# Kernel optimization log

Measured on AMD Instinct MI355X. Metric: run time of the kernel, lower is better.

The kernel has to match this reference:

```python
import jax, jax.numpy as jnp
import numpy as np

B, S, D, H = 4, 2048, 768, 12
HD = D // H  # head_dim = 64


def setup_inputs() -> dict:
    key = jax.random.key(0)
    ks = jax.random.split(key, 5)
    scale = 0.02
    return {
        "x": jax.random.normal(ks[0], (B, S, D), dtype=jnp.float32),
        "wq": jax.random.normal(ks[1], (D, D), dtype=jnp.float32) * scale,
        "wk": jax.random.normal(ks[2], (D, D), dtype=jnp.float32) * scale,
        "wv": jax.random.normal(ks[3], (D, D), dtype=jnp.float32) * scale,
        "wo": jax.random.normal(ks[4], (D, D), dtype=jnp.float32) * scale,
        "bo": jnp.zeros((D,), dtype=jnp.float32),
    }


def reference(x, wq, wk, wv, wo, bo):
    b, s, d = x.shape
    # torch Linear: y = x @ W.T ; qkv_bias=False
    q = (x @ wq.T).reshape(b, s, H, HD).transpose(0, 2, 1, 3)  # [b,h,s,hd]
    k = (x @ wk.T).reshape(b, s, H, HD).transpose(0, 2, 1, 3)
    v = (x @ wv.T).reshape(b, s, H, HD).transpose(0, 2, 1, 3)
    scores = jnp.einsum("bhqd,bhkd->bhqk", q, k)  # full [b,h,s,s] score matrix
    causal = jnp.triu(jnp.ones((s, s), dtype=bool), k=1)
    scores = jnp.where(causal, -jnp.inf, scores)
    attn = jax.nn.softmax(scores / jnp.sqrt(jnp.float32(HD)), axis=-1)
    ctx = jnp.einsum("bhqk,bhkd->bhqd", attn, v)
    ctx = ctx.transpose(0, 2, 1, 3).reshape(b, s, d)
    return ctx @ wo.T + bo  # dropout is identity in eval mode
```

## Files before the change

kernel.cpp:

```cpp
#include <hip/hip_runtime.h>

#define H 12
#define S 2048
#define D 768
#define HD 64
#define BATCH 4
#define M_TOT (BATCH * S)

typedef __attribute__((ext_vector_type(8))) short bf16x8;
typedef __attribute__((ext_vector_type(4))) float f32x4;

__device__ __forceinline__ ushort f2bf(float f) {
  unsigned int x = __float_as_uint(f);
  x += 0x7fffu + ((x >> 16) & 1u);
  return (ushort)(x >> 16);
}

__device__ __forceinline__ uint cvt_pk_bf16(float lo, float hi) {
  uint r;
  asm("v_cvt_pk_bf16_f32 %0, %1, %2" : "=v"(r) : "v"(lo), "v"(hi));
  return r;
}

__device__ __forceinline__ void gload_lds16(const void* gsrc, void* lds) {
  __builtin_amdgcn_global_load_lds(
      (const __attribute__((address_space(1))) unsigned int*)gsrc,
      (__attribute__((address_space(3))) unsigned int*)lds, 16, 0, 0);
}

__global__ __launch_bounds__(256) void cast_all(
    const float* __restrict__ x, const float* __restrict__ wq,
    const float* __restrict__ wk, const float* __restrict__ wv,
    const float* __restrict__ wo, ushort* __restrict__ xb,
    ushort* __restrict__ wqb, ushort* __restrict__ wkb,
    ushort* __restrict__ wvb, ushort* __restrict__ wob) {
  const int NX = M_TOT * D / 4;
  const int NW = D * D / 4;
  int i = blockIdx.x * 256 + threadIdx.x;
  const float* src; ushort* dst; int off;
  if (i < NX) { src = x; dst = xb; off = i; }
  else {
    int j = i - NX; int w = j / NW; off = j - w * NW;
    src = (w == 0) ? wq : (w == 1) ? wk : (w == 2) ? wv : wo;
    dst = (w == 0) ? wqb : (w == 1) ? wkb : (w == 2) ? wvb : wob;
  }
  float4 f = reinterpret_cast<const float4*>(src)[off];
  ushort4 u;
  u.x = f2bf(f.x); u.y = f2bf(f.y); u.z = f2bf(f.z); u.w = f2bf(f.w);
  reinterpret_cast<ushort4*>(dst)[off] = u;
}

__global__ __launch_bounds__(256, 3) void gemm_qkv(
    const ushort* __restrict__ xb, const ushort* __restrict__ wqb,
    const ushort* __restrict__ wkb, const ushort* __restrict__ wvb,
    ushort* __restrict__ qb, ushort* __restrict__ kb_,
    ushort* __restrict__ vtb, float qscale) {
  __shared__ ushort SM[2][10240];
  const int tid = threadIdx.x;
  const int lane = tid & 63, wid = tid >> 6;
  const int g = lane >> 4, li = lane & 15;

  const int wg = blockIdx.x;
  const int mt = wg & 63, slab = wg >> 6;
  const int m0 = mt * 128, n0 = slab * 64;

  const ushort* xm = xb + (size_t)m0 * 768;
  const ushort* wqn = wqb + (size_t)n0 * 768;
  const ushort* wkn = wkb + (size_t)n0 * 768;
  const ushort* wvn = wvb + (size_t)n0 * 768;

  const int rsub = lane >> 2;
  const int coff = (((lane & 3) ^ ((rsub >> 1) & 3)) << 3);
  const int wrow = wid * 16;

  auto stage = [&](int buf, int k0) {
#pragma unroll
    for (int rnd = 0; rnd < 2; ++rnd) {
      const int row0 = rnd * 64 + wrow;
      gload_lds16(&xm[(size_t)(row0 + rsub) * 768 + k0 + coff], &SM[buf][row0 * 32]);
    }
    gload_lds16(&wqn[(size_t)(wrow + rsub) * 768 + k0 + coff], &SM[buf][4096 + wrow * 32]);
    gload_lds16(&wkn[(size_t)(wrow + rsub) * 768 + k0 + coff], &SM[buf][6144 + wrow * 32]);
    gload_lds16(&wvn[(size_t)(wrow + rsub) * 768 + k0 + coff], &SM[buf][8192 + wrow * 32]);
  };

  f32x4 acc[3][2][4] = {};
  stage(0, 0);

  for (int kt = 0; kt < 24; ++kt) {
    const int cur = kt & 1;
    asm volatile("s_waitcnt vmcnt(0)" ::: "memory");
    __syncthreads();
    if (kt + 1 < 24) stage(cur ^ 1, (kt + 1) * 32);

    const ushort* bp = &SM[cur][0];
    bf16x8 a[2];
#pragma unroll
    for (int i = 0; i < 2; ++i) {
      const int row = wid * 32 + i * 16 + li;
      a[i] = *reinterpret_cast<const bf16x8*>(
          &bp[row * 32 + ((g ^ ((row >> 1) & 3)) << 3)]);
    }
#pragma unroll
    for (int o = 0; o < 3; ++o) {
      const int off = 4096 + o * 2048;
      bf16x8 b[4];
#pragma unroll
      for (int j = 0; j < 4; ++j) {
        const int row = j * 16 + li;
        b[j] = *reinterpret_cast<const bf16x8*>(
            &bp[off + row * 32 + ((g ^ ((row >> 1) & 3)) << 3)]);
      }
      __builtin_amdgcn_s_setprio(1);
#pragma unroll
      for (int i = 0; i < 2; ++i)
#pragma unroll
        for (int j = 0; j < 4; ++j)
          acc[o][i][j] = __builtin_amdgcn_mfma_f32_16x16x32_bf16(a[i], b[j], acc[o][i][j], 0, 0, 0);
      __builtin_amdgcn_s_setprio(0);
    }
  }

  ushort* Cs = &SM[0][0];
  const int b0 = m0 >> 11, sb = m0 & 2047;

  __syncthreads();
#pragma unroll
  for (int o = 0; o < 2; ++o)
#pragma unroll
    for (int i = 0; i < 2; ++i)
#pragma unroll
      for (int j = 0; j < 4; ++j)
#pragma unroll
        for (int rr = 0; rr < 4; ++rr) {
          const int row = wid * 32 + i * 16 + g * 4 + rr;
          const int col = j * 16 + li;
          const int pc = ((((col >> 3) ^ (row & 7)) << 3) | (col & 7));
          const float v = acc[o][i][j][rr] * (o == 0 ? qscale : 1.0f);
          Cs[o * 8192 + row * 64 + pc] = f2bf(v);
        }
  __syncthreads();
  {
    const int row = tid >> 1, half = tid & 1;
    const int m = m0 + row;
    const size_t rb = (((size_t)b0 * H + slab) * S + (m & 2047)) * HD + half * 32;
    ushort* dq = &qb[rb];
    ushort* dk = &kb_[rb];
#pragma unroll
    for (int c8 = 0; c8 < 4; ++c8) {
      const int col = half * 32 + c8 * 8;
      const int chunk = (col >> 3) ^ (row & 7);
      *reinterpret_cast<bf16x8*>(&dq[c8 * 8]) =
          *reinterpret_cast<const bf16x8*>(&Cs[row * 64 + chunk * 8]);
      *reinterpret_cast<bf16x8*>(&dk[c8 * 8]) =
          *reinterpret_cast<const bf16x8*>(&Cs[8192 + row * 64 + chunk * 8]);
    }
  }

  __syncthreads();
#pragma unroll
  for (int i = 0; i < 2; ++i)
#pragma unroll
    for (int j = 0; j < 4; ++j)
#pragma unroll
      for (int rr = 0; rr < 4; ++rr) {
        const int tok = wid * 32 + i * 16 + g * 4 + rr;
        const int feat = j * 16 + li;
        const int pc = ((((tok >> 3) ^ (feat & 7)) << 3) | (tok & 7));
        Cs[feat * 128 + pc] = f2bf(acc[2][i][j][rr]);
      }
  __syncthreads();
  {
    const int feat = tid >> 2, qtr = tid & 3;
    ushort* dv = &vtb[(((size_t)b0 * H + slab) * HD + feat) * S + sb + qtr * 32];
#pragma unroll
    for (int c8 = 0; c8 < 4; ++c8) {
      const int tok = qtr * 32 + c8 * 8;
      const int chunk = (tok >> 3) ^ (feat & 7);
      *reinterpret_cast<bf16x8*>(&dv[c8 * 8]) =
          *reinterpret_cast<const bf16x8*>(&Cs[feat * 128 + chunk * 8]);
    }
  }
}

__global__ __launch_bounds__(256) void gemm_wo(const ushort* __restrict__ A,
                                               const ushort* __restrict__ W,
                                               float* __restrict__ out_f,
                                               const float* __restrict__ bias) {
  __shared__ ushort SM[3][6144];
  const int tid = threadIdx.x;
  const int lane = tid & 63, wid = tid >> 6;
  const int g = lane >> 4, li = lane & 15;
  const int wm = wid >> 1, wn = wid & 1;
  const int m0 = blockIdx.x * 64, n0 = blockIdx.y * 128;

  const int rsub = lane >> 2;
  const int coff = (((lane & 3) ^ ((rsub >> 1) & 3)) << 3);

  auto stage = [&](int buf, int k0) {
    gload_lds16(&A[(size_t)(m0 + wid * 16 + rsub) * 768 + k0 + coff],
                &SM[buf][wid * 16 * 32]);
#pragma unroll
    for (int rnd = 0; rnd < 2; ++rnd) {
      const int row0 = rnd * 64 + wid * 16;
      gload_lds16(&W[(size_t)(n0 + row0 + rsub) * 768 + k0 + coff],
                  &SM[buf][2048 + row0 * 32]);
    }
  };

  f32x4 acc[2][4] = {};
  stage(0, 0);
  stage(1, 32);

  int cur = 0, pre = 2;
  for (int kt = 0; kt < 24; ++kt) {
    if (kt < 23) asm volatile("s_waitcnt vmcnt(3) lgkmcnt(0)" ::: "memory");
    else         asm volatile("s_waitcnt vmcnt(0) lgkmcnt(0)" ::: "memory");
    __builtin_amdgcn_s_barrier();
    if (kt + 2 < 24) stage(pre, (kt + 2) * 32);

    bf16x8 a[2], b[4];
#pragma unroll
    for (int i = 0; i < 2; ++i) {
      const int row = wm * 32 + i * 16 + li;
      a[i] = *reinterpret_cast<const bf16x8*>(
          &SM[cur][row * 32 + ((g ^ ((row >> 1) & 3)) << 3)]);
    }
#pragma unroll
    for (int j = 0; j < 4; ++j) {
      const int row = wn * 64 + j * 16 + li;
      b[j] = *reinterpret_cast<const bf16x8*>(
          &SM[cur][2048 + row * 32 + ((g ^ ((row >> 1) & 3)) << 3)]);
    }
    __builtin_amdgcn_s_setprio(1);
#pragma unroll
    for (int i = 0; i < 2; ++i)
#pragma unroll
      for (int j = 0; j < 4; ++j)
        acc[i][j] = __builtin_amdgcn_mfma_f32_16x16x32_bf16(a[i], b[j], acc[i][j], 0, 0, 0);
    __builtin_amdgcn_s_setprio(0);

    cur = (cur == 2) ? 0 : cur + 1;
    pre = (pre == 2) ? 0 : pre + 1;
  }

#pragma unroll
  for (int i = 0; i < 2; ++i)
#pragma unroll
    for (int j = 0; j < 4; ++j)
#pragma unroll
      for (int r = 0; r < 4; ++r) {
        const int m = m0 + wm * 32 + i * 16 + g * 4 + r;
        const int n = n0 + wn * 64 + j * 16 + li;
        out_f[(size_t)m * 768 + n] = acc[i][j][r] + bias[n];
      }
}

__global__ __launch_bounds__(256) void attn_kernel(const ushort* __restrict__ Q,
                                                   const ushort* __restrict__ K,
                                                   const ushort* __restrict__ VT,
                                                   ushort* __restrict__ ctx) {
  __shared__ ushort Ks[2][64 * 64];
  __shared__ ushort Vts[2][64 * 64];
  __shared__ ushort Ps[4][32][72];

  const int tid = threadIdx.x;
  const int lane = tid & 63, wid = tid >> 6;
  const int g = lane >> 4, li = lane & 15;

  const int wg = blockIdx.x;
  const int xcd = wg & 7, t = wg >> 3;
  const int bh = xcd + 8 * (t >> 4);
  const int p = t & 15;
  const int qL = 64 * (31 - p), qS = 64 * p;

  const size_t base = (size_t)bh * S * HD;
  const size_t vtbase = (size_t)bh * HD * S;

  bf16x8 aq[2][2];
#pragma unroll
  for (int f = 0; f < 2; ++f) {
    const size_t qr = base + (size_t)((f ? qS : qL) + wid * 16 + li) * HD;
#pragma unroll
    for (int c = 0; c < 2; ++c)
      aq[f][c] = *reinterpret_cast<const bf16x8*>(&Q[qr + c * 32 + g * 8]);
  }

  f32x4 acc[2][4] = {};
  f32x4 accl[2] = {};
  const uint one2 = 0x3F803F80u;
  uint4 ouv = {one2, one2, one2, one2};
  const bf16x8 ones8 = *reinterpret_cast<const bf16x8*>(&ouv);

  const int nkt = 32 - p;

  const int rsub = lane >> 3;
  const int c8e = (((lane & 7) ^ rsub) << 3);

  auto stage = [&](int buf, int k0) {
#pragma unroll
    for (int rnd = 0; rnd < 2; ++rnd) {
      const int row0 = rnd * 32 + wid * 8;
      gload_lds16(&K[base + (size_t)(k0 + row0 + rsub) * HD + c8e], &Ks[buf][row0 << 6]);
      gload_lds16(&VT[vtbase + (size_t)(row0 + rsub) * S + k0 + c8e], &Vts[buf][row0 << 6]);
    }
  };

  stage(0, 0);

  for (int kt = 0; kt < nkt; ++kt) {
    const int cur = kt & 1;
    const int k0 = kt * 64;
    const bool doS = (kt <= p);

    asm volatile("s_waitcnt vmcnt(0)" ::: "memory");
    __syncthreads();
    if (kt + 1 < nkt) stage(cur ^ 1, k0 + 64);

    f32x4 sc[2][4];
    __builtin_amdgcn_s_setprio(1);
#pragma unroll
    for (int ct = 0; ct < 4; ++ct) {
      const int row = ct * 16 + li, r7 = row & 7;
      const ushort* kr = &Ks[cur][row << 6];
      bf16x8 kb0 = *reinterpret_cast<const bf16x8*>(&kr[(g ^ r7) << 3]);
      bf16x8 kb1 = *reinterpret_cast<const bf16x8*>(&kr[((4 + g) ^ r7) << 3]);
      {
        f32x4 z = {};
        z = __builtin_amdgcn_mfma_f32_16x16x32_bf16(kb0, aq[0][0], z, 0, 0, 0);
        z = __builtin_amdgcn_mfma_f32_16x16x32_bf16(kb1, aq[0][1], z, 0, 0, 0);
        sc[0][ct] = z;
      }
      if (doS) {
        f32x4 z = {};
        z = __builtin_amdgcn_mfma_f32_16x16x32_bf16(kb0, aq[1][0], z, 0, 0, 0);
        z = __builtin_amdgcn_mfma_f32_16x16x32_bf16(kb1, aq[1][1], z, 0, 0, 0);
        sc[1][ct] = z;
      }
    }
    __builtin_amdgcn_s_setprio(0);

    if (kt == nkt - 1) {
      const int q = qL + wid * 16 + li;
#pragma unroll
      for (int ct = 0; ct < 4; ++ct)
#pragma unroll
        for (int r = 0; r < 4; ++r)
          if (k0 + ct * 16 + 4 * g + r > q) sc[0][ct][r] = -1e30f;
    }
    if (kt == p) {
      const int q = qS + wid * 16 + li;
#pragma unroll
      for (int ct = 0; ct < 4; ++ct)
#pragma unroll
        for (int r = 0; r < 4; ++r)
          if (k0 + ct * 16 + 4 * g + r > q) sc[1][ct][r] = -1e30f;
    }

#pragma unroll
    for (int f = 0; f < 2; ++f) {
      if (f == 1 && !doS) break;
#pragma unroll
      for (int ct = 0; ct < 4; ++ct) {
        float p0 = __builtin_amdgcn_exp2f(sc[f][ct][0]);
        float p1 = __builtin_amdgcn_exp2f(sc[f][ct][1]);
        float p2 = __builtin_amdgcn_exp2f(sc[f][ct][2]);
        float p3 = __builtin_amdgcn_exp2f(sc[f][ct][3]);
        uint2 pw;
        pw.x = cvt_pk_bf16(p0, p1);
        pw.y = cvt_pk_bf16(p2, p3);
        *reinterpret_cast<uint2*>(&Ps[wid][f * 16 + li][ct * 16 + 4 * g]) = pw;
      }
    }

    bf16x8 pa[2][2];
    pa[0][0] = *reinterpret_cast<const bf16x8*>(&Ps[wid][li][g * 8]);
    pa[0][1] = *reinterpret_cast<const bf16x8*>(&Ps[wid][li][32 + g * 8]);
    if (doS) {
      pa[1][0] = *reinterpret_cast<const bf16x8*>(&Ps[wid][16 + li][g * 8]);
      pa[1][1] = *reinterpret_cast<const bf16x8*>(&Ps[wid][16 + li][32 + g * 8]);
    }
    __builtin_amdgcn_s_setprio(1);
    accl[0] = __builtin_amdgcn_mfma_f32_16x16x32_bf16(pa[0][0], ones8, accl[0], 0, 0, 0);
    accl[0] = __builtin_amdgcn_mfma_f32_16x16x32_bf16(pa[0][1], ones8, accl[0], 0, 0, 0);
    if (doS) {
      accl[1] = __builtin_amdgcn_mfma_f32_16x16x32_bf16(pa[1][0], ones8, accl[1], 0, 0, 0);
      accl[1] = __builtin_amdgcn_mfma_f32_16x16x32_bf16(pa[1][1], ones8, accl[1], 0, 0, 0);
    }
#pragma unroll
    for (int dt = 0; dt < 4; ++dt) {
      const int row = dt * 16 + li, r7 = row & 7;
      const ushort* vr = &Vts[cur][row << 6];
      bf16x8 vb0 = *reinterpret_cast<const bf16x8*>(&vr[(g ^ r7) << 3]);
      bf16x8 vb1 = *reinterpret_cast<const bf16x8*>(&vr[((4 + g) ^ r7) << 3]);
      acc[0][dt] = __builtin_amdgcn_mfma_f32_16x16x32_bf16(pa[0][0], vb0, acc[0][dt], 0, 0, 0);
      acc[0][dt] = __builtin_amdgcn_mfma_f32_16x16x32_bf16(pa[0][1], vb1, acc[0][dt], 0, 0, 0);
      if (doS) {
        acc[1][dt] = __builtin_amdgcn_mfma_f32_16x16x32_bf16(pa[1][0], vb0, acc[1][dt], 0, 0, 0);
        acc[1][dt] = __builtin_amdgcn_mfma_f32_16x16x32_bf16(pa[1][1], vb1, acc[1][dt], 0, 0, 0);
      }
    }
    __builtin_amdgcn_s_setprio(0);
  }

  const int b = bh / H, h = bh % H;
#pragma unroll
  for (int f = 0; f < 2; ++f) {
#pragma unroll
    for (int r = 0; r < 4; ++r) {
      const float inv = 1.0f / accl[f][r];
      const int s = (f ? qS : qL) + wid * 16 + 4 * g + r;
#pragma unroll
      for (int dt = 0; dt < 4; ++dt)
        ctx[((size_t)(b * S + s)) * D + h * HD + dt * 16 + li] =
            f2bf(acc[f][dt][r] * inv);
    }
  }
}

extern "C" void kernel_launch(void* const* d_in, const int* in_sizes, int n_in,
                              void* d_out, int out_size, void* d_ws, size_t ws_size,
                              hipStream_t stream) {
  (void)in_sizes; (void)n_in; (void)out_size; (void)ws_size;
  const float* x  = (const float*)d_in[0];
  const float* wq = (const float*)d_in[1];
  const float* wk = (const float*)d_in[2];
  const float* wv = (const float*)d_in[3];
  const float* wo = (const float*)d_in[4];
  const float* bo = (const float*)d_in[5];
  float* out = (float*)d_out;

  const size_t xn = (size_t)M_TOT * D;
  const size_t wn = (size_t)D * D;

  ushort* p = (ushort*)d_ws;
  ushort* x_bf  = p; p += xn;
  ushort* wq_bf = p; p += wn;
  ushort* wk_bf = p; p += wn;
  ushort* wv_bf = p; p += wn;
  ushort* wo_bf = p; p += wn;
  ushort* q_bf  = p; p += xn;
  ushort* k_bf  = p; p += xn;
  ushort* vt_bf = p; p += xn;
  ushort* ctx_bf = x_bf;

  cast_all<<<8448, 256, 0, stream>>>(x, wq, wk, wv, wo,
                                     x_bf, wq_bf, wk_bf, wv_bf, wo_bf);

  const float QSCALE = 0.125f * 1.44269504f;
  gemm_qkv<<<768, 256, 0, stream>>>(x_bf, wq_bf, wk_bf, wv_bf,
                                    q_bf, k_bf, vt_bf, QSCALE);

  attn_kernel<<<768, 256, 0, stream>>>(q_bf, k_bf, vt_bf, ctx_bf);

  gemm_wo<<<dim3(128, 6), 256, 0, stream>>>(ctx_bf, wo_bf, out, bo);
}
```

Before: 126.1 us.

## Merge two paired query-tile work items per 512-thread block sharing K/V staging

Attention blocks grow from 4 to 8 waves, and each block handles two adjacent long/short query-tile pairs that share the same K/V tiles staged in LDS. Each wave loads a single 8-row slice per stage instead of two, and waves skip the compute for key tiles beyond their own causal range. The intent is to halve K/V global traffic and staging per unit of work. In exchange, the grid is halved, the waves for the shorter pair sit idle on the final tile, and the P buffer is reused serially per fragment.

```diff
diff --git a/kernel.cpp b/kernel.cpp
--- a/kernel.cpp
+++ b/kernel.cpp
@@ -256,23 +256,31 @@
       }
 }
 
-__global__ __launch_bounds__(256) void attn_kernel(const ushort* __restrict__ Q,
+__global__ __launch_bounds__(512) void attn_kernel(const ushort* __restrict__ Q,
                                                    const ushort* __restrict__ K,
                                                    const ushort* __restrict__ VT,
                                                    ushort* __restrict__ ctx) {
   __shared__ ushort Ks[2][64 * 64];
   __shared__ ushort Vts[2][64 * 64];
-  __shared__ ushort Ps[4][32][72];
+  __shared__ ushort Ps[8][16][72];
 
   const int tid = threadIdx.x;
   const int lane = tid & 63, wid = tid >> 6;
   const int g = lane >> 4, li = lane & 15;
 
   const int wg = blockIdx.x;
-  const int xcd = wg & 7, t = wg >> 3;
-  const int bh = xcd + 8 * (t >> 4);
-  const int p = t & 15;
-  const int qL = 64 * (31 - p), qS = 64 * p;
+  const int xcd = wg & 7;
+  const int rest = wg >> 3;
+  const int headi = rest % 6;
+  const int k2 = rest / 6;
+  const int bh = headi * 8 + xcd;
+
+  const int pA = 2 * k2;
+  const int myp = pA + (wid >> 2);
+  const int qL = 64 * (31 - myp), qS = 64 * myp;
+  const int wr = (wid & 3) * 16;
+  const int myNkt = 32 - myp;
+  const int nkt = 32 - pA;
 
   const size_t base = (size_t)bh * S * HD;
   const size_t vtbase = (size_t)bh * HD * S;
@@ -280,7 +288,7 @@
   bf16x8 aq[2][2];
 #pragma unroll
   for (int f = 0; f < 2; ++f) {
-    const size_t qr = base + (size_t)((f ? qS : qL) + wid * 16 + li) * HD;
+    const size_t qr = base + (size_t)((f ? qS : qL) + wr + li) * HD;
 #pragma unroll
     for (int c = 0; c < 2; ++c)
       aq[f][c] = *reinterpret_cast<const bf16x8*>(&Q[qr + c * 32 + g * 8]);
@@ -292,18 +300,13 @@
   uint4 ouv = {one2, one2, one2, one2};
   const bf16x8 ones8 = *reinterpret_cast<const bf16x8*>(&ouv);
 
-  const int nkt = 32 - p;
-
   const int rsub = lane >> 3;
+  const int srow = wid * 8 + rsub;
   const int c8e = (((lane & 7) ^ rsub) << 3);
 
   auto stage = [&](int buf, int k0) {
-#pragma unroll
-    for (int rnd = 0; rnd < 2; ++rnd) {
-      const int row0 = rnd * 32 + wid * 8;
-      gload_lds16(&K[base + (size_t)(k0 + row0 + rsub) * HD + c8e], &Ks[buf][row0 << 6]);
-      gload_lds16(&VT[vtbase + (size_t)(row0 + rsub) * S + k0 + c8e], &Vts[buf][row0 << 6]);
-    }
+    gload_lds16(&K[base + (size_t)(k0 + srow) * HD + c8e], &Ks[buf][(wid * 8) << 6]);
+    gload_lds16(&VT[vtbase + (size_t)srow * S + k0 + c8e], &Vts[buf][(wid * 8) << 6]);
   };
 
   stage(0, 0);
@@ -311,96 +314,85 @@
   for (int kt = 0; kt < nkt; ++kt) {
     const int cur = kt & 1;
     const int k0 = kt * 64;
-    const bool doS = (kt <= p);
 
     asm volatile("s_waitcnt vmcnt(0)" ::: "memory");
     __syncthreads();
     if (kt + 1 < nkt) stage(cur ^ 1, k0 + 64);
 
-    f32x4 sc[2][4];
-    __builtin_amdgcn_s_setprio(1);
-#pragma unroll
-    for (int ct = 0; ct < 4; ++ct) {
-      const int row = ct * 16 + li, r7 = row & 7;
-      const ushort* kr = &Ks[cur][row << 6];
-      bf16x8 kb0 = *reinterpret_cast<const bf16x8*>(&kr[(g ^ r7) << 3]);
-      bf16x8 kb1 = *reinterpret_cast<const bf16x8*>(&kr[((4 + g) ^ r7) << 3]);
-      {
-        f32x4 z = {};
-        z = __builtin_amdgcn_mfma_f32_16x16x32_bf16(kb0, aq[0][0], z, 0, 0, 0);
-        z = __builtin_amdgcn_mfma_f32_16x16x32_bf16(kb1, aq[0][1], z, 0, 0, 0);
-        sc[0][ct] = z;
-      }
-      if (doS) {
-        f32x4 z = {};
-        z = __builtin_amdgcn_mfma_f32_16x16x32_bf16(kb0, aq[1][0], z, 0, 0, 0);
-        z = __builtin_amdgcn_mfma_f32_16x16x32_bf16(kb1, aq[1][1], z, 0, 0, 0);
-        sc[1][ct] = z;
-      }
-    }
-    __builtin_amdgcn_s_setprio(0);
-
-    if (kt == nkt - 1) {
-      const int q = qL + wid * 16 + li;
-#pragma unroll
-      for (int ct = 0; ct < 4; ++ct)
-#pragma unroll
-        for (int r = 0; r < 4; ++r)
-          if (k0 + ct * 16 + 4 * g + r > q) sc[0][ct][r] = -1e30f;
-    }
-    if (kt == p) {
-      const int q = qS + wid * 16 + li;
-#pragma unroll
-      for (int ct = 0; ct < 4; ++ct)
-#pragma unroll
-        for (int r = 0; r < 4; ++r)
-          if (k0 + ct * 16 + 4 * g + r > q) sc[1][ct][r] = -1e30f;
-    }
-
-#pragma unroll
-    for (int f = 0; f < 2; ++f) {
-      if (f == 1 && !doS) break;
+    if (kt < myNkt) {
+      const bool doS = (kt <= myp);
+
+      f32x4 sc[2][4];
+      __builtin_amdgcn_s_setprio(1);
 #pragma unroll
       for (int ct = 0; ct < 4; ++ct) {
-        float p0 = __builtin_amdgcn_exp2f(sc[f][ct][0]);
-        float p1 = __builtin_amdgcn_exp2f(sc[f][ct][1]);
-        float p2 = __builtin_amdgcn_exp2f(sc[f][ct][2]);
-        float p3 = __builtin_amdgcn_exp2f(sc[f][ct][3]);
-        uint2 pw;
-        pw.x = cvt_pk_bf16(p0, p1);
-        pw.y = cvt_pk_bf16(p2, p3);
-        *reinterpret_cast<uint2*>(&Ps[wid][f * 16 + li][ct * 16 + 4 * g]) = pw;
-      }
-    }
-
-    bf16x8 pa[2][2];
-    pa[0][0] = *reinterpret_cast<const bf16x8*>(&Ps[wid][li][g * 8]);
-    pa[0][1] = *reinterpret_cast<const bf16x8*>(&Ps[wid][li][32 + g * 8]);
-    if (doS) {
-      pa[1][0] = *reinterpret_cast<const bf16x8*>(&Ps[wid][16 + li][g * 8]);
-      pa[1][1] = *reinterpret_cast<const bf16x8*>(&Ps[wid][16 + li][32 + g * 8]);
-    }
-    __builtin_amdgcn_s_setprio(1);
-    accl[0] = __builtin_amdgcn_mfma_f32_16x16x32_bf16(pa[0][0], ones8, accl[0], 0, 0, 0);
-    accl[0] = __builtin_amdgcn_mfma_f32_16x16x32_bf16(pa[0][1], ones8, accl[0], 0, 0, 0);
-    if (doS) {
-      accl[1] = __builtin_amdgcn_mfma_f32_16x16x32_bf16(pa[1][0], ones8, accl[1], 0, 0, 0);
-      accl[1] = __builtin_amdgcn_mfma_f32_16x16x32_bf16(pa[1][1], ones8, accl[1], 0, 0, 0);
-    }
-#pragma unroll
-    for (int dt = 0; dt < 4; ++dt) {
-      const int row = dt * 16 + li, r7 = row & 7;
-      const ushort* vr = &Vts[cur][row << 6];
-      bf16x8 vb0 = *reinterpret_cast<const bf16x8*>(&vr[(g ^ r7) << 3]);
-      bf16x8 vb1 = *reinterpret_cast<const bf16x8*>(&vr[((4 + g) ^ r7) << 3]);
-      acc[0][dt] = __builtin_amdgcn_mfma_f32_16x16x32_bf16(pa[0][0], vb0, acc[0][dt], 0, 0, 0);
-      acc[0][dt] = __builtin_amdgcn_mfma_f32_16x16x32_bf16(pa[0][1], vb1, acc[0][dt], 0, 0, 0);
-      if (doS) {
-        acc[1][dt] = __builtin_amdgcn_mfma_f32_16x16x32_bf16(pa[1][0], vb0, acc[1][dt], 0, 0, 0);
-        acc[1][dt] = __builtin_amdgcn_mfma_f32_16x16x32_bf16(pa[1][1], vb1, acc[1][dt], 0, 0, 0);
-      }
-    }
-    __builtin_amdgcn_s_setprio(0);
+        const int row = ct * 16 + li, r7 = row & 7;
+        const ushort* kr = &Ks[cur][row << 6];
+        bf16x8 kb0 = *reinterpret_cast<const bf16x8*>(&kr[(g ^ r7) << 3]);
+        bf16x8 kb1 = *reinterpret_cast<const bf16x8*>(&kr[((4 + g) ^ r7) << 3]);
+        {
+          f32x4 z = {};
+          z = __builtin_amdgcn_mfma_f32_16x16x32_bf16(kb0, aq[0][0], z, 0, 0, 0);
+          z = __builtin_amdgcn_mfma_f32_16x16x32_bf16(kb1, aq[0][1], z, 0, 0, 0);
+          sc[0][ct] = z;
+        }
+        if (doS) {
+          f32x4 z = {};
+          z = __builtin_amdgcn_mfma_f32_16x16x32_bf16(kb0, aq[1][0], z, 0, 0, 0);
+          z = __builtin_amdgcn_mfma_f32_16x16x32_bf16(kb1, aq[1][1], z, 0, 0, 0);
+          sc[1][ct] = z;
+        }
+      }
+      __builtin_amdgcn_s_setprio(0);
+
+      if (kt == myNkt - 1) {
+        const int q = qL + wr + li;
+#pragma unroll
+        for (int ct = 0; ct < 4; ++ct)
+#pragma unroll
+          for (int r = 0; r < 4; ++r)
+            if (k0 + ct * 16 + 4 * g + r > q) sc[0][ct][r] = -1e30f;
+      }
+      if (kt == myp) {
+        const int q = qS + wr + li;
+#pragma unroll
+        for (int ct = 0; ct < 4; ++ct)
+#pragma unroll
+          for (int r = 0; r < 4; ++r)
+            if (k0 + ct * 16 + 4 * g + r > q) sc[1][ct][r] = -1e30f;
+      }
+
+#pragma unroll
+      for (int f = 0; f < 2; ++f) {
+        if (f == 1 && !doS) break;
+#pragma unroll
+        for (int ct = 0; ct < 4; ++ct) {
+          float p0 = __builtin_amdgcn_exp2f(sc[f][ct][0]);
+          float p1 = __builtin_amdgcn_exp2f(sc[f][ct][1]);
+          float p2 = __builtin_amdgcn_exp2f(sc[f][ct][2]);
+          float p3 = __builtin_amdgcn_exp2f(sc[f][ct][3]);
+          uint2 pw;
+          pw.x = cvt_pk_bf16(p0, p1);
+          pw.y = cvt_pk_bf16(p2, p3);
+          *reinterpret_cast<uint2*>(&Ps[wid][li][ct * 16 + 4 * g]) = pw;
+        }
+        bf16x8 pa0 = *reinterpret_cast<const bf16x8*>(&Ps[wid][li][g * 8]);
+        bf16x8 pa1 = *reinterpret_cast<const bf16x8*>(&Ps[wid][li][32 + g * 8]);
+        __builtin_amdgcn_s_setprio(1);
+        accl[f] = __builtin_amdgcn_mfma_f32_16x16x32_bf16(pa0, ones8, accl[f], 0, 0, 0);
+        accl[f] = __builtin_amdgcn_mfma_f32_16x16x32_bf16(pa1, ones8, accl[f], 0, 0, 0);
+#pragma unroll
+        for (int dt = 0; dt < 4; ++dt) {
+          const int row = dt * 16 + li, r7 = row & 7;
+          const ushort* vr = &Vts[cur][row << 6];
+          bf16x8 vb0 = *reinterpret_cast<const bf16x8*>(&vr[(g ^ r7) << 3]);
+          bf16x8 vb1 = *reinterpret_cast<const bf16x8*>(&vr[((4 + g) ^ r7) << 3]);
+          acc[f][dt] = __builtin_amdgcn_mfma_f32_16x16x32_bf16(pa0, vb0, acc[f][dt], 0, 0, 0);
+          acc[f][dt] = __builtin_amdgcn_mfma_f32_16x16x32_bf16(pa1, vb1, acc[f][dt], 0, 0, 0);
+        }
+        __builtin_amdgcn_s_setprio(0);
+      }
+    }
   }
 
   const int b = bh / H, h = bh % H;
@@ -409,7 +401,7 @@
 #pragma unroll
     for (int r = 0; r < 4; ++r) {
       const float inv = 1.0f / accl[f][r];
-      const int s = (f ? qS : qL) + wid * 16 + 4 * g + r;
+      const int s = (f ? qS : qL) + wr + 4 * g + r;
 #pragma unroll
       for (int dt = 0; dt < 4; ++dt)
         ctx[((size_t)(b * S + s)) * D + h * HD + dt * 16 + li] =
@@ -451,7 +443,7 @@
   gemm_qkv<<<768, 256, 0, stream>>>(x_bf, wq_bf, wk_bf, wv_bf,
                                     q_bf, k_bf, vt_bf, QSCALE);
 
-  attn_kernel<<<768, 256, 0, stream>>>(q_bf, k_bf, vt_bf, ctx_bf);
+  attn_kernel<<<384, 512, 0, stream>>>(q_bf, k_bf, vt_bf, ctx_bf);
 
   gemm_wo<<<dim3(128, 6), 256, 0, stream>>>(ctx_bf, wo_bf, out, bo);
 }
```

Result: faster. 122.0 us, median of 2 (-3.2%).
